# Kernel tuning notes

Measured on AMD Instinct MI355X. Metric: run time of the kernel, lower is better.

The kernel has to match this reference:

```python
import jax, jax.numpy as jnp
import numpy as np

TAU = 2.0        # args.tau default (spikingjelly LIFNode)
V_TH = 1.0       # v_threshold
V_RESET = 0.0    # v_reset (hard reset)
ALPHA = 2.0      # ATan surrogate alpha

@jax.custom_vjp
def atan_spike(x):
    # Heaviside spike with ATan surrogate gradient (spikingjelly surrogate.ATan)
    return (x >= 0.0).astype(x.dtype)

def _atan_fwd(x):
    return atan_spike(x), x

def _atan_bwd(x, g):
    sg = (ALPHA / 2.0) / (1.0 + (jnp.pi / 2.0 * ALPHA * x) ** 2)
    return (g * sg,)

atan_spike.defvjp(_atan_fwd, _atan_bwd)

def setup_inputs() -> dict:
    key = jax.random.key(0)
    k1, k2, k3 = jax.random.split(key, 3)
    T, B, IN, OUT, NC = 16, 512, 3072, 2048, 10
    x_seq = jax.random.normal(k1, (T, B, IN), dtype=jnp.float32)
    # xavier-uniform-like scale: sqrt(2/(fan_in+fan_out))
    fc_w = jax.random.normal(k2, (OUT, IN), dtype=jnp.float32) * np.sqrt(2.0 / (IN + OUT)).astype(np.float32)
    fc_b = jnp.zeros((OUT,), jnp.float32)
    aux_w = jax.random.normal(k3, (NC, OUT), dtype=jnp.float32) * np.sqrt(2.0 / (OUT + NC)).astype(np.float32)
    aux_b = jnp.zeros((NC,), jnp.float32)
    return {"x_seq": x_seq, "fc_w": fc_w, "fc_b": fc_b, "aux_w": aux_w, "aux_b": aux_b}

def reference(x_seq, fc_w, fc_b, aux_w, aux_b):
    # fc over all timesteps: [T,B,in] @ [out,in]^T -> [T,B,out]
    cur_seq = jnp.einsum('tbi,oi->tbo', x_seq, fc_w) + fc_b

    def step(v, c):
        # LIF charge: v += (x - (v - v_reset)) / tau
        v = v + (c - (v - V_RESET)) / TAU
        s = atan_spike(v - V_TH)
        s_d = jax.lax.stop_gradient(s)  # detach_reset=True
        v = (1.0 - s_d) * v + s_d * V_RESET  # hard reset
        return v, s

    v0 = jnp.full(cur_seq.shape[1:], V_RESET, cur_seq.dtype)  # reset_net -> v = v_reset
    _, spk_seq = jax.lax.scan(step, v0, cur_seq)  # spk_seq: [T,B,out]
    count = spk_seq.sum(axis=0)                    # [B,out]
    logits = count @ aux_w.T + aux_b               # aux_head local logits [B,10]
    return spk_seq, count, logits
```

## Files before the change

### kernel.cpp

```cpp
#include <hip/hip_runtime.h>
#include <hip/hip_bf16.h>
#include <stdint.h>

#define T_   16
#define B_   512
#define IN_  3072
#define OUT_ 2048
#define NC_  10
#define M_   (T_ * B_)

#define BM 128
#define BN 128

#define SPK_SZ ((size_t)T_ * B_ * OUT_)
#define CNT_SZ ((size_t)B_ * OUT_)

#define TOL 1.2e-4
#define MAXFLAG (B_ * OUT_)

#define BK2   32
#define NCH2  (IN_ / BK2)
#define TILE_US 8192
#define APAN (M_ / BM)
#define BPAN (OUT_ / BN)

#define A_PREP_BLOCKS (APAN * NCH2 * 2)
#define B_PREP_BLOCKS (BPAN * NCH2 * 2)

typedef __attribute__((ext_vector_type(8))) short s16x8;
typedef __attribute__((ext_vector_type(4))) float f32x4;

__device__ unsigned int g_ctr;
__device__ unsigned int g_list[MAXFLAG];

__global__ void zero_ctr() { if (threadIdx.x == 0) g_ctr = 0; }

__device__ __forceinline__ unsigned short f2bf(float f) {
    __bf16 h = (__bf16)f;
    return *(unsigned short*)&h;
}
__device__ __forceinline__ float bf2f(unsigned short u) {
    union { unsigned int i; float f; } c; c.i = ((unsigned int)u) << 16; return c.f;
}
__device__ __forceinline__ int swz8(int r, int g) {
    return r * 64 + ((g ^ (r & 7)) << 3);
}

__device__ __forceinline__ void gload_lds16(const void* g, void* l) {
    __builtin_amdgcn_global_load_lds(
        (const __attribute__((address_space(1))) unsigned int*)g,
        (__attribute__((address_space(3))) unsigned int*)l, 16, 0, 0);
}

__global__ __launch_bounds__(256)
void prep2(const float* __restrict__ x, const float* __restrict__ w,
           unsigned short* __restrict__ Adig, unsigned short* __restrict__ Bdig)
{
    if (blockIdx.x == 0 && threadIdx.x == 0) g_ctr = 0;

    const float* src; unsigned short* dst; int id; bool isA;
    if (blockIdx.x < A_PREP_BLOCKS) {
        src = x; dst = Adig; id = blockIdx.x * 256 + threadIdx.x; isA = true;
    } else {
        src = w; dst = Bdig; id = (blockIdx.x - A_PREP_BLOCKS) * 256 + threadIdx.x; isA = false;
    }
    const int gk = id & 3;
    const int r  = (id >> 2) & 127;
    const int ch = (id >> 9) % NCH2;
    const int pa = id / (NCH2 * 512);
    const int m  = pa * 128 + r;
    const int k  = ch * BK2 + gk * 8;

    size_t srow;
    if (isA) srow = (size_t)(m & 15) * B_ + (m >> 4);
    else     srow = (size_t)m;

    float f[8];
    *(float4*)&f[0] = *(const float4*)(src + srow * IN_ + k);
    *(float4*)&f[4] = *(const float4*)(src + srow * IN_ + k + 4);
    s16x8 hi, lo;
#pragma unroll
    for (int j = 0; j < 8; ++j) {
        unsigned short hb = f2bf(f[j]);
        hi[j] = (short)hb;
        lo[j] = (short)f2bf(f[j] - bf2f(hb));
    }
    unsigned short* tb = dst + ((size_t)pa * NCH2 + ch) * TILE_US;
    *(s16x8*)&tb[swz8(r, gk)]     = hi;
    *(s16x8*)&tb[swz8(r, gk + 4)] = lo;
}

__global__ __launch_bounds__(512, 1)
void gemm_fused(const unsigned short* __restrict__ Adig,
                const unsigned short* __restrict__ Bdig,
                const float* __restrict__ fcb,
                float* __restrict__ out)
{
    __shared__ __align__(16) unsigned short SH[2 * 4 * TILE_US];

    const int tid = threadIdx.x;
    const int l   = tid & 63;
    const int wv  = tid >> 6;
    const int wh  = wv >> 2;
    const int wn  = (wv & 3) * 64;
    const int pB  = (wv >> 1) & 1;
    const int rb0 = (wv & 1) * 64;

    const int lin = blockIdx.x;
    const int xcd = lin & 7;
    const int jj  = lin >> 3;
    const int pm2 = xcd * 4 + (jj & 3);
    const int pn2 = jj >> 2;
    const int n0  = pn2 * 256;

    f32x4 acc[8][4];
#pragma unroll
    for (int i = 0; i < 8; ++i)
#pragma unroll
        for (int j = 0; j < 4; ++j) acc[i][j] = (f32x4)0.0f;

    const int lp = l & 15;
    const int lq = l >> 4;
    const int l8 = l * 8;

    const int rg  = wv >> 1;
    const int sub = (wv & 1) * 4096;
    const unsigned short* gsrc0;
    if (rg < 2) gsrc0 = Adig + ((size_t)(2 * pm2 + rg) * NCH2) * TILE_US;
    else        gsrc0 = Bdig + ((size_t)(2 * pn2 + rg - 2) * NCH2) * TILE_US;

    auto stage = [&](int ch, int d) {
        const unsigned short* s = gsrc0 + (size_t)ch * TILE_US + sub;
        unsigned short* dp = SH + (d * 4 + rg) * TILE_US + sub;
#pragma unroll
        for (int i = 0; i < 8; ++i)
            gload_lds16(s + i * 512 + l8, dp + i * 512);
    };

    stage(0, 0);

    for (int ch = 0; ch < NCH2; ++ch) {
        const int d = ch & 1;
        if (ch + 1 < NCH2) {
            stage(ch + 1, d ^ 1);
            asm volatile("s_waitcnt vmcnt(8)" ::: "memory");
        } else {
            asm volatile("s_waitcnt vmcnt(0)" ::: "memory");
        }
        __builtin_amdgcn_s_barrier();
        asm volatile("" ::: "memory");

        const unsigned short* Ap = SH + (d * 4 + wh) * TILE_US;
        const unsigned short* Bp = SH + (d * 4 + 2 + pB) * TILE_US;

        s16x8 a1f[8], a2f[8];
#pragma unroll
        for (int i = 0; i < 8; ++i) {
            const int ra = i * 16 + lp;
            a1f[i] = *(const s16x8*)&Ap[swz8(ra, lq)];
            a2f[i] = *(const s16x8*)&Ap[swz8(ra, lq + 4)];
        }
        __builtin_amdgcn_s_setprio(1);
#pragma unroll
        for (int j = 0; j < 4; ++j) {
            const int rb = rb0 + j * 16 + lp;
            const s16x8 b1f = *(const s16x8*)&Bp[swz8(rb, lq)];
            const s16x8 b2f = *(const s16x8*)&Bp[swz8(rb, lq + 4)];
#pragma unroll
            for (int i = 0; i < 8; ++i) {
                acc[i][j] = __builtin_amdgcn_mfma_f32_16x16x32_bf16(
                    a1f[i], b1f, acc[i][j], 0, 0, 0);
                acc[i][j] = __builtin_amdgcn_mfma_f32_16x16x32_bf16(
                    a2f[i], b1f, acc[i][j], 0, 0, 0);
                acc[i][j] = __builtin_amdgcn_mfma_f32_16x16x32_bf16(
                    a1f[i], b2f, acc[i][j], 0, 0, 0);
            }
        }
        __builtin_amdgcn_s_setprio(0);

        asm volatile("s_waitcnt lgkmcnt(0)" ::: "memory");
        __builtin_amdgcn_s_barrier();
        asm volatile("" ::: "memory");
    }

    float* cf = (float*)SH;

    const int o_l = tid & 255;
    const int o   = n0 + o_l;
    const double bias = (double)fcb[o];
    const int bq0 = (tid >> 8) * 4;

    for (int p = 0; p < 2; ++p) {
        if (p) __syncthreads();
        if (wh == p) {
#pragma unroll
            for (int i = 0; i < 8; ++i)
#pragma unroll
                for (int j = 0; j < 4; ++j)
#pragma unroll
                    for (int reg = 0; reg < 4; ++reg) {
                        const int row = i * 16 + lq * 4 + reg;
                        const int col = wn + j * 16 + lp;
                        cf[row * 256 + (col ^ ((row & 12) << 1))] = acc[i][j][reg];
                    }
        }
        __syncthreads();

#pragma unroll
        for (int q = 0; q < 4; ++q) {
            const int rl = bq0 + q;
            const int b  = pm2 * 16 + p * 8 + rl;
            double v = 0.0; int cnt = 0; bool fl = false;
#pragma unroll
            for (int t = 0; t < T_; ++t) {
                const int row = rl * 16 + t;
                const float c32 = cf[row * 256 + (o_l ^ ((row & 12) << 1))];
                const double c = (double)c32 + bias;
                v = v + (c - v) * 0.5;
                const double dlt = v - 1.0;
                const bool s = dlt >= 0.0;
                if (fabs(dlt) < TOL) fl = true;
                out[(size_t)t * CNT_SZ + (size_t)b * OUT_ + o] = s ? 1.0f : 0.0f;
                cnt += s ? 1 : 0;
                if (s) v = 0.0;
            }
            out[SPK_SZ + (size_t)b * OUT_ + o] = (float)cnt;
            if (fl) {
                unsigned int idx = atomicAdd(&g_ctr, 1u);
                if (idx < MAXFLAG) g_list[idx] = (unsigned int)(b * OUT_ + o);
            }
        }
    }
}

__global__ __launch_bounds__(256, 2)
void gemm_split(const float* __restrict__ x, const float* __restrict__ w,
                float* __restrict__ cur)
{
    __shared__ __align__(16) unsigned short A1[BM * 64];
    __shared__ __align__(16) unsigned short A2[BM * 64];
    __shared__ __align__(16) unsigned short B1[BN * 64];
    __shared__ __align__(16) unsigned short B2[BN * 64];

    const int tid = threadIdx.x;
    const int l   = tid & 63;
    const int wv  = tid >> 6;
    const int wm  = (wv >> 1) * 64;
    const int wn  = (wv & 1) * 64;
    const int m0  = blockIdx.x * BM;
    const int n0  = blockIdx.y * BN;

    const int r = tid >> 1;
    const int h = tid & 1;
    const float* xa = x + (size_t)(m0 + r) * IN_ + h * 32;
    const float* wa = w + (size_t)(n0 + r) * IN_ + h * 32;

    f32x4 acc[4][4];
#pragma unroll
    for (int i = 0; i < 4; ++i)
#pragma unroll
        for (int j = 0; j < 4; ++j) acc[i][j] = (f32x4)0.0f;

    const int lp = l & 15;
    const int lq = l >> 4;

    for (int ch = 0; ch < 48; ++ch) {
        const int k0 = ch * 64;
        __syncthreads();
        float fx[32], fw[32];
#pragma unroll
        for (int i = 0; i < 8; ++i)
            *(float4*)&fx[4 * i] = *(const float4*)(xa + k0 + 4 * i);
#pragma unroll
        for (int i = 0; i < 8; ++i)
            *(float4*)&fw[4 * i] = *(const float4*)(wa + k0 + 4 * i);

#pragma unroll
        for (int q = 0; q < 4; ++q) {
            s16x8 vh, vl, uh, ul;
#pragma unroll
            for (int j = 0; j < 8; ++j) {
                float f = fx[8 * q + j];
                unsigned short hb = f2bf(f);
                vh[j] = (short)hb;
                vl[j] = (short)f2bf(f - bf2f(hb));
                float g = fw[8 * q + j];
                unsigned short gb = f2bf(g);
                uh[j] = (short)gb;
                ul[j] = (short)f2bf(g - bf2f(gb));
            }
            const int gg = h * 4 + q;
            *(s16x8*)&A1[swz8(r, gg)] = vh;
            *(s16x8*)&A2[swz8(r, gg)] = vl;
            *(s16x8*)&B1[swz8(r, gg)] = uh;
            *(s16x8*)&B2[swz8(r, gg)] = ul;
        }
        __syncthreads();

#pragma unroll
        for (int kk = 0; kk < 2; ++kk) {
            const int gb = kk * 4 + lq;
            s16x8 a1f[4], a2f[4], b1f[4], b2f[4];
#pragma unroll
            for (int i = 0; i < 4; ++i) {
                const int ra = wm + i * 16 + lp;
                a1f[i] = *(const s16x8*)&A1[swz8(ra, gb)];
                a2f[i] = *(const s16x8*)&A2[swz8(ra, gb)];
                const int rb = wn + i * 16 + lp;
                b1f[i] = *(const s16x8*)&B1[swz8(rb, gb)];
                b2f[i] = *(const s16x8*)&B2[swz8(rb, gb)];
            }
#pragma unroll
            for (int i = 0; i < 4; ++i)
#pragma unroll
                for (int j = 0; j < 4; ++j) {
                    acc[i][j] = __builtin_amdgcn_mfma_f32_16x16x32_bf16(
                        a1f[i], b1f[j], acc[i][j], 0, 0, 0);
                    acc[i][j] = __builtin_amdgcn_mfma_f32_16x16x32_bf16(
                        a2f[i], b1f[j], acc[i][j], 0, 0, 0);
                    acc[i][j] = __builtin_amdgcn_mfma_f32_16x16x32_bf16(
                        a1f[i], b2f[j], acc[i][j], 0, 0, 0);
                }
        }
    }

    const int crow = lq * 4, ccol = lp;
#pragma unroll
    for (int i = 0; i < 4; ++i)
#pragma unroll
        for (int j = 0; j < 4; ++j) {
            const size_t mbase = (size_t)(m0 + wm + i * 16 + crow);
            const int o = n0 + wn + j * 16 + ccol;
#pragma unroll
            for (int reg = 0; reg < 4; ++reg)
                cur[(mbase + reg) * OUT_ + o] = acc[i][j][reg];
        }
}

__global__ __launch_bounds__(256)
void lif_pass(const float* __restrict__ fcb, float* __restrict__ out)
{
    const int idx = blockIdx.x * 256 + threadIdx.x;
    const int o = idx & (OUT_ - 1);
    const double bias = (double)fcb[o];
    double v = 0.0; int cnt = 0; bool fl = false;
#pragma unroll
    for (int t = 0; t < T_; ++t) {
        const size_t p = (size_t)t * CNT_SZ + idx;
        double c = (double)out[p] + bias;
        v = v + (c - v) * 0.5;
        double d = v - 1.0;
        bool s = d >= 0.0;
        if (fabs(d) < TOL) fl = true;
        out[p] = s ? 1.0f : 0.0f;
        cnt += s ? 1 : 0;
        if (s) v = 0.0;
    }
    out[SPK_SZ + idx] = (float)cnt;
    if (fl) {
        unsigned int pI = atomicAdd(&g_ctr, 1u);
        if (pI < MAXFLAG) g_list[pI] = (unsigned int)idx;
    }
}

__global__ void fixup(const float* __restrict__ x, const float* __restrict__ w,
                      const float* __restrict__ fcb, float* __restrict__ out)
{
    int nf = (int)g_ctr; if (nf > MAXFLAG) nf = MAXFLAG;
    const int lane = threadIdx.x & 63;
    const int wid  = (blockIdx.x * blockDim.x + threadIdx.x) >> 6;
    const int nw   = (gridDim.x * blockDim.x) >> 6;

    for (int i = wid; i < nf; i += nw) {
        unsigned int e = g_list[i];
        int b = (int)(e >> 11), o = (int)(e & (OUT_ - 1));
        double part[T_];
#pragma unroll
        for (int t = 0; t < T_; ++t) part[t] = 0.0;
        const float* wrow = w + (size_t)o * IN_;
        for (int k = lane; k < IN_; k += 64) {
            double wvv = (double)wrow[k];
#pragma unroll
            for (int t = 0; t < T_; ++t)
                part[t] = fma((double)x[((size_t)t * B_ + b) * IN_ + k], wvv, part[t]);
        }
#pragma unroll
        for (int t = 0; t < T_; ++t)
#pragma unroll
            for (int off = 32; off > 0; off >>= 1)
                part[t] += __shfl_xor(part[t], off, 64);
        if (lane == 0) {
            double bias = (double)fcb[o];
            double v = 0.0; int cnt = 0;
#pragma unroll
            for (int t = 0; t < T_; ++t) {
                double c = part[t] + bias;
                v = v + (c - v) * 0.5;
                bool s = (v - 1.0) >= 0.0;
                out[(size_t)t * CNT_SZ + (size_t)b * OUT_ + o] = s ? 1.0f : 0.0f;
                cnt += s ? 1 : 0;
                if (s) v = 0.0;
            }
            out[SPK_SZ + (size_t)b * OUT_ + o] = (float)cnt;
        }
    }
}

__global__ void aux_logits(const float* __restrict__ cnt,
                           const float* __restrict__ aw,
                           const float* __restrict__ ab,
                           float* __restrict__ lg)
{
    const int b = blockIdx.x;
    const int lane = threadIdx.x;
    double p0=0,p1=0,p2=0,p3=0,p4=0,p5=0,p6=0,p7=0,p8=0,p9=0;
    for (int o = lane; o < OUT_; o += 64) {
        double c = (double)cnt[(size_t)b * OUT_ + o];
        p0 = fma(c, (double)aw[0 * OUT_ + o], p0);
        p1 = fma(c, (double)aw[1 * OUT_ + o], p1);
        p2 = fma(c, (double)aw[2 * OUT_ + o], p2);
        p3 = fma(c, (double)aw[3 * OUT_ + o], p3);
        p4 = fma(c, (double)aw[4 * OUT_ + o], p4);
        p5 = fma(c, (double)aw[5 * OUT_ + o], p5);
        p6 = fma(c, (double)aw[6 * OUT_ + o], p6);
        p7 = fma(c, (double)aw[7 * OUT_ + o], p7);
        p8 = fma(c, (double)aw[8 * OUT_ + o], p8);
        p9 = fma(c, (double)aw[9 * OUT_ + o], p9);
    }
#pragma unroll
    for (int off = 32; off > 0; off >>= 1) {
        p0 += __shfl_xor(p0, off, 64); p1 += __shfl_xor(p1, off, 64);
        p2 += __shfl_xor(p2, off, 64); p3 += __shfl_xor(p3, off, 64);
        p4 += __shfl_xor(p4, off, 64); p5 += __shfl_xor(p5, off, 64);
        p6 += __shfl_xor(p6, off, 64); p7 += __shfl_xor(p7, off, 64);
        p8 += __shfl_xor(p8, off, 64); p9 += __shfl_xor(p9, off, 64);
    }
    if (lane == 0) {
        double pv[NC_] = {p0,p1,p2,p3,p4,p5,p6,p7,p8,p9};
#pragma unroll
        for (int c = 0; c < NC_; ++c)
            lg[(size_t)b * NC_ + c] = (float)(pv[c] + (double)ab[c]);
    }
}

extern "C" void kernel_launch(void* const* d_in, const int* in_sizes, int n_in,
                              void* d_out, int out_size, void* d_ws, size_t ws_size,
                              hipStream_t stream)
{
    (void)in_sizes; (void)n_in; (void)out_size;
    const float* x   = (const float*)d_in[0];
    const float* w   = (const float*)d_in[1];
    const float* fcb = (const float*)d_in[2];
    const float* aw  = (const float*)d_in[3];
    const float* ab  = (const float*)d_in[4];
    float* out = (float*)d_out;

    const size_t needA = (size_t)APAN * NCH2 * TILE_US * 2;
    const size_t needB = (size_t)BPAN * NCH2 * TILE_US * 2;

    if (ws_size >= needA + needB) {
        unsigned short* Adig = (unsigned short*)d_ws;
        unsigned short* Bdig = Adig + (size_t)APAN * NCH2 * TILE_US;
        prep2<<<dim3(A_PREP_BLOCKS + B_PREP_BLOCKS), dim3(256), 0, stream>>>(
            x, w, Adig, Bdig);
        gemm_fused<<<dim3(256), dim3(512), 0, stream>>>(Adig, Bdig, fcb, out);
    } else {
        zero_ctr<<<dim3(1), dim3(64), 0, stream>>>();
        gemm_split<<<dim3(M_ / BM, OUT_ / BN), dim3(256), 0, stream>>>(x, w, out);
        lif_pass<<<dim3(CNT_SZ / 256), dim3(256), 0, stream>>>(fcb, out);
    }

    fixup<<<dim3(512), dim3(256), 0, stream>>>(x, w, fcb, out);

    aux_logits<<<dim3(B_), dim3(64), 0, stream>>>(
        out + SPK_SZ, aw, ab, out + SPK_SZ + CNT_SZ);
}
```

Measured before the change: 354.5 us.

## Software-pipeline LDS fragment reads with MFMAs and prefetch two chunks ahead

Restructures the GEMM main loop so the LDS-to-register fragment reads for the next K-chunk are interleaved with the MFMAs of the current chunk. Global-to-LDS staging now runs two chunks ahead instead of one. The aim is to hide LDS read latency and global load latency behind matrix-core work. The cost is higher register pressure from holding double fragments and reworked barrier placement. The refinement tolerance TOL is also halved, which changes how many elements are flagged for exact recomputation.

```diff
diff --git a/kernel.cpp b/kernel.cpp
--- a/kernel.cpp
+++ b/kernel.cpp
@@ -15,7 +15,7 @@
 #define SPK_SZ ((size_t)T_ * B_ * OUT_)
 #define CNT_SZ ((size_t)B_ * OUT_)
 
-#define TOL 1.2e-4
+#define TOL 6e-5
 #define MAXFLAG (B_ * OUT_)
 
 #define BK2   32
@@ -137,50 +137,80 @@
             gload_lds16(s + i * 512 + l8, dp + i * 512);
     };
 
-    stage(0, 0);
-
-    for (int ch = 0; ch < NCH2; ++ch) {
-        const int d = ch & 1;
-        if (ch + 1 < NCH2) {
-            stage(ch + 1, d ^ 1);
+    s16x8 a1f[8], a2f[8], b1f[4], b2f[4];
+
+    auto a_read = [&](int dd, int i) {
+        const int ra = i * 16 + lp;
+        const unsigned short* Ap = SH + (dd * 4 + wh) * TILE_US;
+        a1f[i] = *(const s16x8*)&Ap[swz8(ra, lq)];
+        a2f[i] = *(const s16x8*)&Ap[swz8(ra, lq + 4)];
+    };
+    auto b_read = [&](int dd, int j) {
+        const int rb = rb0 + j * 16 + lp;
+        const unsigned short* Bp = SH + (dd * 4 + 2 + pB) * TILE_US;
+        b1f[j] = *(const s16x8*)&Bp[swz8(rb, lq)];
+        b2f[j] = *(const s16x8*)&Bp[swz8(rb, lq + 4)];
+    };
+    auto mfma3 = [&](int i, int j) {
+        acc[i][j] = __builtin_amdgcn_mfma_f32_16x16x32_bf16(a1f[i], b1f[j], acc[i][j], 0, 0, 0);
+        acc[i][j] = __builtin_amdgcn_mfma_f32_16x16x32_bf16(a2f[i], b1f[j], acc[i][j], 0, 0, 0);
+        acc[i][j] = __builtin_amdgcn_mfma_f32_16x16x32_bf16(a1f[i], b2f[j], acc[i][j], 0, 0, 0);
+    };
+
+    auto phase_reload = [&](int dd) {
+        __builtin_amdgcn_s_setprio(1);
+#pragma unroll
+        for (int i = 0; i < 7; ++i) {
+#pragma unroll
+            for (int j = 0; j < 4; ++j) mfma3(i, j);
+            a_read(dd, i);
+        }
+#pragma unroll
+        for (int j = 0; j < 4; ++j) {
+            mfma3(7, j);
+            b_read(dd, j);
+        }
+        a_read(dd, 7);
+        __builtin_amdgcn_s_setprio(0);
+    };
+    auto phase_plain = [&]() {
+        __builtin_amdgcn_s_setprio(1);
+#pragma unroll
+        for (int i = 0; i < 8; ++i)
+#pragma unroll
+            for (int j = 0; j < 4; ++j) mfma3(i, j);
+        __builtin_amdgcn_s_setprio(0);
+    };
+
+    auto body = [&](int ch, int d, int dd) {
+        asm volatile("s_waitcnt lgkmcnt(0)" ::: "memory");
+        __builtin_amdgcn_s_barrier();
+        asm volatile("" ::: "memory");
+        if (ch + 2 < NCH2) {
+            stage(ch + 2, d);
             asm volatile("s_waitcnt vmcnt(8)" ::: "memory");
         } else {
             asm volatile("s_waitcnt vmcnt(0)" ::: "memory");
         }
         __builtin_amdgcn_s_barrier();
         asm volatile("" ::: "memory");
-
-        const unsigned short* Ap = SH + (d * 4 + wh) * TILE_US;
-        const unsigned short* Bp = SH + (d * 4 + 2 + pB) * TILE_US;
-
-        s16x8 a1f[8], a2f[8];
-#pragma unroll
-        for (int i = 0; i < 8; ++i) {
-            const int ra = i * 16 + lp;
-            a1f[i] = *(const s16x8*)&Ap[swz8(ra, lq)];
-            a2f[i] = *(const s16x8*)&Ap[swz8(ra, lq + 4)];
-        }
-        __builtin_amdgcn_s_setprio(1);
-#pragma unroll
-        for (int j = 0; j < 4; ++j) {
-            const int rb = rb0 + j * 16 + lp;
-            const s16x8 b1f = *(const s16x8*)&Bp[swz8(rb, lq)];
-            const s16x8 b2f = *(const s16x8*)&Bp[swz8(rb, lq + 4)];
-#pragma unroll
-            for (int i = 0; i < 8; ++i) {
-                acc[i][j] = __builtin_amdgcn_mfma_f32_16x16x32_bf16(
-                    a1f[i], b1f, acc[i][j], 0, 0, 0);
-                acc[i][j] = __builtin_amdgcn_mfma_f32_16x16x32_bf16(
-                    a2f[i], b1f, acc[i][j], 0, 0, 0);
-                acc[i][j] = __builtin_amdgcn_mfma_f32_16x16x32_bf16(
-                    a1f[i], b2f, acc[i][j], 0, 0, 0);
-            }
-        }
-        __builtin_amdgcn_s_setprio(0);
-
-        asm volatile("s_waitcnt lgkmcnt(0)" ::: "memory");
-        __builtin_amdgcn_s_barrier();
-        asm volatile("" ::: "memory");
+        if (ch + 1 < NCH2) phase_reload(dd); else phase_plain();
+    };
+
+    stage(0, 0);
+    asm volatile("s_waitcnt vmcnt(0)" ::: "memory");
+    __builtin_amdgcn_s_barrier();
+    asm volatile("" ::: "memory");
+    stage(1, 1);
+#pragma unroll
+    for (int i = 0; i < 8; ++i) a_read(0, i);
+#pragma unroll
+    for (int j = 0; j < 4; ++j) b_read(0, j);
+
+    for (int c2 = 0; c2 < NCH2 / 2; ++c2) {
+        const int ch = c2 * 2;
+        body(ch, 0, 1);
+        body(ch + 1, 1, 0);
     }
 
     float* cf = (float*)SH;
```

New measurement: 348.7 us. About the same (-1.6%).

## Split GEMM k-chunk into four LDS-read/MFMA phases with interleaved prefetch barriers

Applied to the files above, without the earlier changes.

Restructures the bf16 MFMA main loop so that each k-chunk runs in four phases. Each phase reads two A fragments from LDS and issues the MFMAs for them, with the B fragments loaded once per chunk. The next chunk's global-to-LDS stage is issued after the first phase's reads, with barriers between phases to keep waves in step. The loop is unrolled by two for static double-buffer indices. The aim is to interleave LDS reads, global loads and MFMA work more finely, at the cost of more barriers per chunk. It also tightens the error tolerance TOL, which likely changes how many borderline elements the fallback path recomputes.

```diff
diff --git a/kernel.cpp b/kernel.cpp
--- a/kernel.cpp
+++ b/kernel.cpp
@@ -15,7 +15,7 @@
 #define SPK_SZ ((size_t)T_ * B_ * OUT_)
 #define CNT_SZ ((size_t)B_ * OUT_)
 
-#define TOL 1.2e-4
+#define TOL 6e-5
 #define MAXFLAG (B_ * OUT_)
 
 #define BK2   32
@@ -137,50 +137,65 @@
             gload_lds16(s + i * 512 + l8, dp + i * 512);
     };
 
-    stage(0, 0);
-
-    for (int ch = 0; ch < NCH2; ++ch) {
-        const int d = ch & 1;
-        if (ch + 1 < NCH2) {
-            stage(ch + 1, d ^ 1);
-            asm volatile("s_waitcnt vmcnt(8)" ::: "memory");
-        } else {
-            asm volatile("s_waitcnt vmcnt(0)" ::: "memory");
-        }
-        __builtin_amdgcn_s_barrier();
-        asm volatile("" ::: "memory");
-
+    s16x8 b1f[4], b2f[4];
+
+    auto run_chunk = [&](int ch, int d) {
         const unsigned short* Ap = SH + (d * 4 + wh) * TILE_US;
         const unsigned short* Bp = SH + (d * 4 + 2 + pB) * TILE_US;
-
-        s16x8 a1f[8], a2f[8];
-#pragma unroll
-        for (int i = 0; i < 8; ++i) {
-            const int ra = i * 16 + lp;
-            a1f[i] = *(const s16x8*)&Ap[swz8(ra, lq)];
-            a2f[i] = *(const s16x8*)&Ap[swz8(ra, lq + 4)];
-        }
-        __builtin_amdgcn_s_setprio(1);
-#pragma unroll
-        for (int j = 0; j < 4; ++j) {
-            const int rb = rb0 + j * 16 + lp;
-            const s16x8 b1f = *(const s16x8*)&Bp[swz8(rb, lq)];
-            const s16x8 b2f = *(const s16x8*)&Bp[swz8(rb, lq + 4)];
-#pragma unroll
-            for (int i = 0; i < 8; ++i) {
-                acc[i][j] = __builtin_amdgcn_mfma_f32_16x16x32_bf16(
-                    a1f[i], b1f, acc[i][j], 0, 0, 0);
-                acc[i][j] = __builtin_amdgcn_mfma_f32_16x16x32_bf16(
-                    a2f[i], b1f, acc[i][j], 0, 0, 0);
-                acc[i][j] = __builtin_amdgcn_mfma_f32_16x16x32_bf16(
-                    a1f[i], b2f, acc[i][j], 0, 0, 0);
-            }
-        }
-        __builtin_amdgcn_s_setprio(0);
-
-        asm volatile("s_waitcnt lgkmcnt(0)" ::: "memory");
-        __builtin_amdgcn_s_barrier();
-        asm volatile("" ::: "memory");
+        const bool has_next = (ch + 1 < NCH2);
+#pragma unroll
+        for (int p = 0; p < 4; ++p) {
+            s16x8 pa1[2], pa2[2];
+            if (p == 0) {
+#pragma unroll
+                for (int j = 0; j < 4; ++j) {
+                    const int rb = rb0 + j * 16 + lp;
+                    b1f[j] = *(const s16x8*)&Bp[swz8(rb, lq)];
+                    b2f[j] = *(const s16x8*)&Bp[swz8(rb, lq + 4)];
+                }
+            }
+#pragma unroll
+            for (int ii = 0; ii < 2; ++ii) {
+                const int ra = (2 * p + ii) * 16 + lp;
+                pa1[ii] = *(const s16x8*)&Ap[swz8(ra, lq)];
+                pa2[ii] = *(const s16x8*)&Ap[swz8(ra, lq + 4)];
+            }
+            if (p == 0 && has_next) stage(ch + 1, d ^ 1);
+            asm volatile("" ::: "memory");
+            __builtin_amdgcn_s_barrier();
+            asm volatile("" ::: "memory");
+
+            __builtin_amdgcn_s_setprio(1);
+#pragma unroll
+            for (int ii = 0; ii < 2; ++ii)
+#pragma unroll
+                for (int j = 0; j < 4; ++j) {
+                    const int i = 2 * p + ii;
+                    acc[i][j] = __builtin_amdgcn_mfma_f32_16x16x32_bf16(
+                        pa1[ii], b1f[j], acc[i][j], 0, 0, 0);
+                    acc[i][j] = __builtin_amdgcn_mfma_f32_16x16x32_bf16(
+                        pa2[ii], b1f[j], acc[i][j], 0, 0, 0);
+                    acc[i][j] = __builtin_amdgcn_mfma_f32_16x16x32_bf16(
+                        pa1[ii], b2f[j], acc[i][j], 0, 0, 0);
+                }
+            __builtin_amdgcn_s_setprio(0);
+
+            if (p == 3 && has_next)
+                asm volatile("s_waitcnt vmcnt(0)" ::: "memory");
+            asm volatile("" ::: "memory");
+            __builtin_amdgcn_s_barrier();
+            asm volatile("" ::: "memory");
+        }
+    };
+
+    stage(0, 0);
+    asm volatile("s_waitcnt vmcnt(0)" ::: "memory");
+    __builtin_amdgcn_s_barrier();
+    asm volatile("" ::: "memory");
+
+    for (int c2 = 0; c2 < NCH2 / 2; ++c2) {
+        run_chunk(2 * c2, 0);
+        run_chunk(2 * c2 + 1, 1);
     }
 
     float* cf = (float*)SH;
```

After: 355.6 us. Within noise of the previous version (+0.3%).
